# Kernel tuning notes

Measured on AMD Instinct MI355X. Metric: run time of the kernel, lower is better.

The kernel has to match this reference:

```python
import jax, jax.numpy as jnp
import numpy as np

D = 1024       # d_model
S = 32         # n_slots
EMA = 0.05     # slot_ema (alpha)
RSCALE = 1.0   # read_logit_scale
LN_EPS = 1e-5


def setup_inputs() -> dict:
    key = jax.random.key(0)
    ks = jax.random.split(key, 6)
    B, T = 2, 2048
    h = jax.random.normal(ks[0], (B, T, D), jnp.float32)
    # init_batched_memory_state: small random slots
    state0 = jax.random.normal(ks[1], (B, S, D), jnp.float32) * 0.01
    # xavier_uniform for (out=D, in=D) Linear weights, zero bias
    bound = float(np.sqrt(6.0 / (D + D)))
    Wq = jax.random.uniform(ks[2], (D, D), jnp.float32, -bound, bound)
    Wv = jax.random.uniform(ks[3], (D, D), jnp.float32, -bound, bound)
    bq = jnp.zeros((D,), jnp.float32)
    bv = jnp.zeros((D,), jnp.float32)
    ln_gamma = jnp.ones((D,), jnp.float32)
    ln_beta = jnp.zeros((D,), jnp.float32)
    return {"h": h, "state0": state0, "ln_gamma": ln_gamma, "ln_beta": ln_beta,
            "Wq": Wq, "bq": bq, "Wv": Wv, "bv": bv, "chunk_size": 128}


def _layer_norm(x, gamma, beta):
    mu = jnp.mean(x, axis=-1, keepdims=True)
    var = jnp.mean(jnp.square(x - mu), axis=-1, keepdims=True)
    return (x - mu) * jax.lax.rsqrt(var + LN_EPS) * gamma + beta


def reference(h, state0, ln_gamma, ln_beta, Wq, bq, Wv, bv, chunk_size):
    """write_parallel (soft-routed EMA prefix-scan write) followed by
    read_parallel (per-token softmax slot attention). Returns (ctx, final_state)."""
    B, T, d = h.shape
    alpha = EMA
    a = 1.0 - alpha
    h_norm = _layer_norm(h, ln_gamma, ln_beta)                  # (B,T,d)
    v = h_norm @ Wv.T + bv                                      # value_proj
    q = h_norm @ Wq.T + bq                                      # query_proj
    scale = RSCALE * d ** (-0.5)
    # routing weights from queries vs initial state (breaks seq dependency)
    scores = jnp.einsum('btd,bsd->bts', q, state0) * scale       # (B,T,S)
    w = jax.nn.softmax(scores, axis=-1)
    u = alpha * w[..., None] * v[:, :, None, :]                  # (B,T,S,d)

    n_chunks = T // chunk_size
    Cn = chunk_size
    u_chunks = u.reshape(B, n_chunks, Cn, S, d).transpose(1, 0, 2, 3, 4)
    t_idx = jnp.arange(Cn, dtype=h.dtype)
    decay = a ** t_idx                                           # (Cn,)
    inv_decay = 1.0 / jnp.clip(decay, 1e-30)
    t1_decay = a ** (t_idx + 1.0)

    def step(state, u_c):  # state (B,S,d), u_c (B,Cn,S,d)
        cs = jnp.cumsum(u_c * inv_decay[None, :, None, None], axis=1)
        chunk_states = (decay[None, :, None, None] * cs
                        + t1_decay[None, :, None, None] * state[:, None])
        return chunk_states[:, -1], chunk_states

    final_state, states = jax.lax.scan(step, state0, u_chunks)
    states = states.transpose(1, 0, 2, 3, 4).reshape(B, T, S, d)  # (B,T,S,d)

    # read_parallel: softmax slot attention per token against its own state
    scores_r = jnp.einsum('btd,btsd->bts', q, states) * scale
    attn = jax.nn.softmax(scores_r, axis=-1)
    ctx = jnp.einsum('bts,btsd->btd', attn, states)               # (B,T,d)
    return ctx, final_state
```

## Files before the change

kernel.cpp:

```cpp
#include <hip/hip_runtime.h>

#define Bn 2
#define Tn 2048
#define Dn 1024
#define Sn 32
#define CH 64
#define NCH 32
#define ALPHA 0.05f
#define Adec 0.95f
#define SCALE 0.03125f

typedef __attribute__((ext_vector_type(8))) __bf16 bf16x8;
typedef __attribute__((ext_vector_type(4))) __bf16 bf16x4;
typedef __attribute__((ext_vector_type(4))) float f32x4;

__device__ __forceinline__ void async_copy16(const void* g, void* l) {
  __builtin_amdgcn_global_load_lds(
      (const __attribute__((address_space(1))) unsigned int*)g,
      (__attribute__((address_space(3))) unsigned int*)l, 16, 0, 0);
}

__device__ __forceinline__ bool is_bf16(const void* gam) {
  return ((const unsigned short*)gam)[0] == 0x3F80u;
}

#define W8 (Dn * Dn / 8)
#define S8 (Bn * Sn * Dn / 8)
__global__ __launch_bounds__(256) void conv_k(
    const void* __restrict__ Wq, const void* __restrict__ Wv,
    const void* __restrict__ s0, const void* __restrict__ gam,
    __bf16* __restrict__ Wqb, __bf16* __restrict__ Wvb, __bf16* __restrict__ s0b) {
  bool isb = is_bf16(gam);
  int g = blockIdx.x * 256 + threadIdx.x;
  const void* src; __bf16* dst; int off;
  if (g < W8)            { src = Wq; dst = Wqb; off = g; }
  else if (g < 2 * W8)   { src = Wv; dst = Wvb; off = g - W8; }
  else                   { src = s0; dst = s0b; off = g - 2 * W8; }
  if (isb) {
    *(bf16x8*)&dst[(size_t)off * 8] = ((const bf16x8*)src)[off];
  } else {
    const float* s = (const float*)src + (size_t)off * 8;
    f32x4 a = *(const f32x4*)s, b = *(const f32x4*)(s + 4);
    bf16x8 t;
    t[0] = (__bf16)a[0]; t[1] = (__bf16)a[1]; t[2] = (__bf16)a[2]; t[3] = (__bf16)a[3];
    t[4] = (__bf16)b[0]; t[5] = (__bf16)b[1]; t[6] = (__bf16)b[2]; t[7] = (__bf16)b[3];
    *(bf16x8*)&dst[(size_t)off * 8] = t;
  }
}

__global__ __launch_bounds__(256) void ln_k(const void* __restrict__ hp,
    const void* __restrict__ gp, const void* __restrict__ bp,
    __bf16* __restrict__ hn) {
  int row = blockIdx.x;
  int tid = threadIdx.x;
  bool isb = is_bf16(gp);
  float x0, x1, x2, x3;
  if (isb) {
    const __bf16* x = (const __bf16*)hp + (size_t)row * Dn;
    bf16x4 xv = *(const bf16x4*)&x[tid * 4];
    x0 = (float)xv[0]; x1 = (float)xv[1]; x2 = (float)xv[2]; x3 = (float)xv[3];
  } else {
    const float* x = (const float*)hp + (size_t)row * Dn;
    f32x4 xv = *(const f32x4*)&x[tid * 4];
    x0 = xv[0]; x1 = xv[1]; x2 = xv[2]; x3 = xv[3];
  }
  float s  = x0 + x1 + x2 + x3;
  float s2 = x0*x0 + x1*x1 + x2*x2 + x3*x3;
  #pragma unroll
  for (int m = 32; m >= 1; m >>= 1) { s += __shfl_xor(s, m); s2 += __shfl_xor(s2, m); }
  __shared__ float red[8];
  int wave = tid >> 6, lane = tid & 63;
  if (lane == 0) { red[wave] = s; red[4 + wave] = s2; }
  __syncthreads();
  s  = red[0] + red[1] + red[2] + red[3];
  s2 = red[4] + red[5] + red[6] + red[7];
  float mu  = s * (1.0f / Dn);
  float var = s2 * (1.0f / Dn) - mu * mu;
  float rs  = rsqrtf(var + 1e-5f);
  float g0, g1, g2, g3, be0, be1, be2, be3;
  if (isb) {
    bf16x4 gv = *(const bf16x4*)&((const __bf16*)gp)[tid * 4];
    bf16x4 bv = *(const bf16x4*)&((const __bf16*)bp)[tid * 4];
    g0 = (float)gv[0]; g1 = (float)gv[1]; g2 = (float)gv[2]; g3 = (float)gv[3];
    be0 = (float)bv[0]; be1 = (float)bv[1]; be2 = (float)bv[2]; be3 = (float)bv[3];
  } else {
    f32x4 gv = *(const f32x4*)&((const float*)gp)[tid * 4];
    f32x4 bv = *(const f32x4*)&((const float*)bp)[tid * 4];
    g0 = gv[0]; g1 = gv[1]; g2 = gv[2]; g3 = gv[3];
    be0 = bv[0]; be1 = bv[1]; be2 = bv[2]; be3 = bv[3];
  }
  bf16x4 o;
  o[0] = (__bf16)((x0 - mu) * rs * g0 + be0);
  o[1] = (__bf16)((x1 - mu) * rs * g1 + be1);
  o[2] = (__bf16)((x2 - mu) * rs * g2 + be2);
  o[3] = (__bf16)((x3 - mu) * rs * g3 + be3);
  *(bf16x4*)&hn[(size_t)row * Dn + tid * 4] = o;
}

__global__ __launch_bounds__(256) void gemm_qv_k(
    const __bf16* __restrict__ A,
    const __bf16* __restrict__ Wqb, const void* __restrict__ bqp,
    const __bf16* __restrict__ Wvb, const void* __restrict__ bvp,
    const void* __restrict__ gam,
    __bf16* __restrict__ Qo, __bf16* __restrict__ Vo) {
  const int K = Dn, N = Dn;
  bool isb = is_bf16(gam);
  int mt = blockIdx.x & 31;
  int ng = blockIdx.x >> 5;
  const __bf16* W; const void* biasp; __bf16* O; int nt;
  if (ng < 8) { W = Wqb; biasp = bqp; O = Qo; nt = ng; }
  else        { W = Wvb; biasp = bvp; O = Vo; nt = ng - 8; }
  int m0 = mt * 128, n0 = nt * 128;
  __shared__ alignas(16) __bf16 lA[128 * 64];
  __shared__ alignas(16) __bf16 lB[128 * 64];
  int tid = threadIdx.x, lane = tid & 63, wave = tid >> 6;
  int wm = (wave >> 1) * 64, wn = (wave & 1) * 64;
  int lm = lane & 15, q8 = (lane >> 4) * 8;
  f32x4 zero4 = {0.f, 0.f, 0.f, 0.f};
  f32x4 acc[4][4];
  #pragma unroll
  for (int i = 0; i < 4; ++i)
    #pragma unroll
    for (int j = 0; j < 4; ++j) acc[i][j] = zero4;

  for (int k0 = 0; k0 < K; k0 += 64) {
    __syncthreads();
    #pragma unroll
    for (int r = 0; r < 4; ++r) {
      int idx = r * 256 + tid;
      int row = idx >> 3, c8 = (idx & 7) * 8;
      async_copy16(&A[(size_t)(m0 + row) * K + k0 + c8], &lA[idx * 8]);
      async_copy16(&W[(size_t)(n0 + row) * K + k0 + c8], &lB[idx * 8]);
    }
    __syncthreads();
    #pragma unroll
    for (int kk = 0; kk < 64; kk += 32) {
      bf16x8 af[4], bfr[4];
      #pragma unroll
      for (int i = 0; i < 4; ++i) {
        af[i]  = *(const bf16x8*)&lA[(wm + i * 16 + lm) * 64 + kk + q8];
        bfr[i] = *(const bf16x8*)&lB[(wn + i * 16 + lm) * 64 + kk + q8];
      }
      #pragma unroll
      for (int i = 0; i < 4; ++i)
        #pragma unroll
        for (int j = 0; j < 4; ++j)
          acc[i][j] = __builtin_amdgcn_mfma_f32_16x16x32_bf16(af[i], bfr[j], acc[i][j], 0, 0, 0);
    }
  }
  int r4 = (lane >> 4) * 4;
  #pragma unroll
  for (int j = 0; j < 4; ++j) {
    int colN = n0 + wn + j * 16 + lm;
    float bb = isb ? (float)((const __bf16*)biasp)[colN] : ((const float*)biasp)[colN];
    #pragma unroll
    for (int i = 0; i < 4; ++i) {
      int row0 = m0 + wm + i * 16 + r4;
      #pragma unroll
      for (int r = 0; r < 4; ++r)
        O[(size_t)(row0 + r) * N + colN] = (__bf16)(acc[i][j][r] + bb);
    }
  }
}

#define SP 33
__global__ __launch_bounds__(256) void router_k(const __bf16* __restrict__ qb,
    const __bf16* __restrict__ s0b, float* __restrict__ wbuf) {
  int tokBase = blockIdx.x * 64;
  int b = tokBase >> 11;
  const __bf16* S = s0b + (size_t)b * Sn * Dn;
  __shared__ alignas(16) __bf16 lQ[64 * 64];
  __shared__ alignas(16) __bf16 lS[Sn * 64];
  __shared__ float fSc[64 * SP];
  int tid = threadIdx.x, lane = tid & 63, wave = tid >> 6;
  int lm = lane & 15, q8 = (lane >> 4) * 8;
  f32x4 zero4 = {0.f, 0.f, 0.f, 0.f};
  f32x4 acc[2]; acc[0] = zero4; acc[1] = zero4;

  for (int k0 = 0; k0 < Dn; k0 += 64) {
    __syncthreads();
    #pragma unroll
    for (int r = 0; r < 2; ++r) {
      int idx = r * 256 + tid;
      async_copy16(&qb[(size_t)(tokBase + (idx >> 3)) * Dn + k0 + (idx & 7) * 8], &lQ[idx * 8]);
    }
    async_copy16(&S[(size_t)(tid >> 3) * Dn + k0 + (tid & 7) * 8], &lS[tid * 8]);
    __syncthreads();
    #pragma unroll
    for (int kk = 0; kk < 64; kk += 32) {
      bf16x8 af = *(const bf16x8*)&lQ[(wave * 16 + lm) * 64 + kk + q8];
      #pragma unroll
      for (int j = 0; j < 2; ++j) {
        bf16x8 bb = *(const bf16x8*)&lS[(j * 16 + lm) * 64 + kk + q8];
        acc[j] = __builtin_amdgcn_mfma_f32_16x16x32_bf16(af, bb, acc[j], 0, 0, 0);
      }
    }
  }
  int r4 = (lane >> 4) * 4;
  #pragma unroll
  for (int j = 0; j < 2; ++j)
    #pragma unroll
    for (int r = 0; r < 4; ++r)
      fSc[(wave * 16 + r4 + r) * SP + j * 16 + lm] = acc[j][r];
  __syncthreads();
  if (tid < 64) {
    int t = tid;
    float mx = -1e30f;
    #pragma unroll
    for (int s = 0; s < Sn; ++s) mx = fmaxf(mx, fSc[t * SP + s]);
    float sum = 0.f;
    float ex[Sn];
    #pragma unroll
    for (int s = 0; s < Sn; ++s) { ex[s] = __expf(fSc[t * SP + s] * SCALE - mx * SCALE); sum += ex[s]; }
    float inv = 1.f / sum;
    #pragma unroll
    for (int s = 0; s < Sn; ++s)
      wbuf[(size_t)(tokBase + t) * Sn + s] = ex[s] * inv;
  }
}

__global__ __launch_bounds__(256) void contrib_k(const __bf16* __restrict__ v,
    const float* __restrict__ wbuf, float* __restrict__ contrib) {
  int blk = blockIdx.x;
  int bc = blk >> 2, dq = blk & 3;
  int b = bc >> 5, c = bc & 31;
  int tokBase = b * Tn + c * CH;
  int d0 = dq * 256;
  __shared__ alignas(16) float coef[CH * Sn];
  __shared__ float dp[CH];
  int tid = threadIdx.x;
  if (tid < CH) dp[tid] = powf(Adec, (float)(CH - 1 - tid));
  __syncthreads();
  for (int i = tid; i < CH * Sn; i += 256) {
    int j = i >> 5;
    coef[i] = ALPHA * dp[j] * wbuf[(size_t)tokBase * Sn + i];
  }
  __syncthreads();
  int st = tid >> 6;
  int dg = tid & 63;
  int d4 = d0 + dg * 4;
  int sb = st * 8;
  f32x4 zero4 = {0.f, 0.f, 0.f, 0.f};
  f32x4 acc[8];
  #pragma unroll
  for (int i = 0; i < 8; ++i) acc[i] = zero4;
  for (int j = 0; j < CH; ++j) {
    bf16x4 vv = *(const bf16x4*)&v[(size_t)(tokBase + j) * Dn + d4];
    f32x4 vf = {(float)vv[0], (float)vv[1], (float)vv[2], (float)vv[3]};
    f32x4 c0 = *(const f32x4*)&coef[j * Sn + sb];
    f32x4 c1 = *(const f32x4*)&coef[j * Sn + sb + 4];
    acc[0] += vf * c0[0]; acc[1] += vf * c0[1]; acc[2] += vf * c0[2]; acc[3] += vf * c0[3];
    acc[4] += vf * c1[0]; acc[5] += vf * c1[1]; acc[6] += vf * c1[2]; acc[7] += vf * c1[3];
  }
  float* outp = contrib + (size_t)bc * Sn * Dn;
  #pragma unroll
  for (int i = 0; i < 8; ++i)
    *(f32x4*)&outp[(size_t)(sb + i) * Dn + d4] = acc[i];
}

__global__ __launch_bounds__(256) void scan_k(const void* __restrict__ s0p,
    const float* __restrict__ contrib, const void* __restrict__ gam,
    __bf16* __restrict__ S0b, void* __restrict__ outp) {
  int idx = blockIdx.x * 256 + threadIdx.x;
  bool isb = is_bf16(gam);
  int b = idx >> 15, sd = idx & 32767;
  float val = isb ? (float)((const __bf16*)s0p)[idx] : ((const float*)s0p)[idx];
  const float aC = powf(Adec, (float)CH);
  #pragma unroll 8
  for (int c = 0; c < NCH; ++c) {
    size_t off = ((size_t)(b * NCH + c) << 15) + sd;
    S0b[off] = (__bf16)val;
    val = aC * val + contrib[off];
  }
  size_t fsbase = (size_t)Bn * Tn * Dn;
  if (isb) ((__bf16*)outp)[fsbase + idx] = (__bf16)val;
  else     ((float*)outp)[fsbase + idx] = val;
}

__global__ __launch_bounds__(256) void attn_k(
    const __bf16* __restrict__ q, const __bf16* __restrict__ v,
    const float* __restrict__ wbuf, const __bf16* __restrict__ S0b,
    float* __restrict__ Pbuf, float* __restrict__ A2buf) {
  int bc = blockIdx.x;
  int b = bc >> 5, c = bc & 31;
  int tokBase = b * Tn + c * CH;
  const __bf16* S0c = S0b + (size_t)bc * Sn * Dn;

  __shared__ alignas(16) __bf16 lQ[CH * 64];
  __shared__ alignas(16) __bf16 lV[CH * 64];
  __shared__ alignas(16) __bf16 lS[Sn * 64];
  __shared__ alignas(16) __bf16 lM[CH * 72];
  __shared__ alignas(16) __bf16 lW[CH * 40];
  __shared__ alignas(16) __bf16 lWt[Sn * 72];
  __shared__ alignas(16) __bf16 lAt[CH * 40];
  __shared__ float dp[CH + 1];

  int tid = threadIdx.x, lane = tid & 63, wave = tid >> 6;
  int lm = lane & 15, q8 = (lane >> 4) * 8;
  int r4 = (lane >> 4) * 4;
  f32x4 zero4 = {0.f, 0.f, 0.f, 0.f};
  f32x4 aQV[4], aQS[2];
  #pragma unroll
  for (int i = 0; i < 4; ++i) aQV[i] = zero4;
  aQS[0] = zero4; aQS[1] = zero4;

  for (int i = tid; i < CH * Sn; i += 256) {
    int j = i >> 5, s = i & 31;
    __bf16 wb = (__bf16)wbuf[(size_t)tokBase * Sn + i];
    lW[j * 40 + s] = wb;
    lWt[s * 72 + j] = wb;
  }
  if (tid < CH + 1) dp[tid] = powf(Adec, (float)tid);

  for (int k0 = 0; k0 < Dn; k0 += 64) {
    __syncthreads();
    #pragma unroll
    for (int r = 0; r < 2; ++r) {
      int idx = r * 256 + tid;
      int row = idx >> 3, c8 = (idx & 7) * 8;
      async_copy16(&q[(size_t)(tokBase + row) * Dn + k0 + c8], &lQ[idx * 8]);
      async_copy16(&v[(size_t)(tokBase + row) * Dn + k0 + c8], &lV[idx * 8]);
    }
    async_copy16(&S0c[(size_t)(tid >> 3) * Dn + k0 + (tid & 7) * 8], &lS[tid * 8]);
    __syncthreads();
    #pragma unroll
    for (int kk = 0; kk < 64; kk += 32) {
      bf16x8 af = *(const bf16x8*)&lQ[(wave * 16 + lm) * 64 + kk + q8];
      #pragma unroll
      for (int j = 0; j < 4; ++j) {
        bf16x8 bb = *(const bf16x8*)&lV[(j * 16 + lm) * 64 + kk + q8];
        aQV[j] = __builtin_amdgcn_mfma_f32_16x16x32_bf16(af, bb, aQV[j], 0, 0, 0);
      }
      #pragma unroll
      for (int j = 0; j < 2; ++j) {
        bf16x8 bb = *(const bf16x8*)&lS[(j * 16 + lm) * 64 + kk + q8];
        aQS[j] = __builtin_amdgcn_mfma_f32_16x16x32_bf16(af, bb, aQS[j], 0, 0, 0);
      }
    }
  }

  #pragma unroll
  for (int jt = 0; jt < 4; ++jt)
    #pragma unroll
    for (int r = 0; r < 4; ++r) {
      int t = wave * 16 + r4 + r, j = jt * 16 + lm;
      float f = (j <= t) ? ALPHA * dp[t - j] : 0.0f;
      lM[t * 72 + j] = (__bf16)(aQV[jt][r] * f);
    }

  f32x4 sc[2]; sc[0] = zero4; sc[1] = zero4;
  #pragma unroll
  for (int kt = 0; kt < 2; ++kt) {
    bf16x8 am = *(const bf16x8*)&lM[(wave * 16 + lm) * 72 + kt * 32 + q8];
    #pragma unroll
    for (int st = 0; st < 2; ++st) {
      bf16x8 bb = *(const bf16x8*)&lWt[(st * 16 + lm) * 72 + kt * 32 + q8];
      sc[st] = __builtin_amdgcn_mfma_f32_16x16x32_bf16(am, bb, sc[st], 0, 0, 0);
    }
  }
  float at0[4], at1[4];
  #pragma unroll
  for (int r = 0; r < 4; ++r) {
    int t = wave * 16 + r4 + r;
    float aQ = dp[t - wave * 16 + 1 + wave * 16];
    float s0v = SCALE * (aQ * aQS[0][r] + sc[0][r]);
    float s1v = SCALE * (aQ * aQS[1][r] + sc[1][r]);
    float mx = fmaxf(s0v, s1v);
    #pragma unroll
    for (int m = 8; m >= 1; m >>= 1) mx = fmaxf(mx, __shfl_xor(mx, m));
    float e0 = __expf(s0v - mx), e1 = __expf(s1v - mx);
    float su = e0 + e1;
    #pragma unroll
    for (int m = 8; m >= 1; m >>= 1) su += __shfl_xor(su, m);
    float inv = 1.f / su;
    at0[r] = e0 * inv; at1[r] = e1 * inv;
    A2buf[(size_t)bc * CH * Sn + t * Sn + lm]      = aQ * at0[r];
    A2buf[(size_t)bc * CH * Sn + t * Sn + 16 + lm] = aQ * at1[r];
    lAt[t * 40 + lm]      = (__bf16)at0[r];
    lAt[t * 40 + 16 + lm] = (__bf16)at1[r];
  }
  bf16x8 aa = *(const bf16x8*)&lAt[(wave * 16 + lm) * 40 + q8];
  #pragma unroll
  for (int jt = 0; jt < 4; ++jt) {
    bf16x8 bb = *(const bf16x8*)&lW[(jt * 16 + lm) * 40 + q8];
    f32x4 pj = __builtin_amdgcn_mfma_f32_16x16x32_bf16(aa, bb, zero4, 0, 0, 0);
    #pragma unroll
    for (int r = 0; r < 4; ++r) {
      int t = wave * 16 + r4 + r, j = jt * 16 + lm;
      float val = (j <= t) ? ALPHA * dp[t - j] * pj[r] : 0.0f;
      Pbuf[(size_t)bc * CH * CH + t * CH + j] = val;
    }
  }
}

__global__ __launch_bounds__(256) void ctx_k(const __bf16* __restrict__ v,
    const __bf16* __restrict__ S0b, const float* __restrict__ Pbuf,
    const float* __restrict__ A2buf, const void* __restrict__ gam,
    void* __restrict__ ctxp) {
  int blk = blockIdx.x;
  int bc = blk >> 3, dt = blk & 7;
  int b = bc >> 5, c = bc & 31;
  int tokBase = b * Tn + c * CH;
  int d0 = dt * 128;
  bool isb = is_bf16(gam);
  __shared__ alignas(16) float lP[CH * CH];
  __shared__ alignas(16) float lA2[CH * Sn];
  __shared__ alignas(16) __bf16 lV[CH * 128];
  __shared__ alignas(16) __bf16 lS[Sn * 128];
  int tid = threadIdx.x;
  {
    const f32x4* src = (const f32x4*)(Pbuf + (size_t)bc * CH * CH);
    f32x4* dst = (f32x4*)lP;
    for (int i = tid; i < CH * CH / 4; i += 256) dst[i] = src[i];
    const f32x4* src2 = (const f32x4*)(A2buf + (size_t)bc * CH * Sn);
    f32x4* dst2 = (f32x4*)lA2;
    for (int i = tid; i < CH * Sn / 4; i += 256) dst2[i] = src2[i];
    for (int i = tid; i < CH * 128 / 8; i += 256) {
      int j = i >> 4, dd = (i & 15) * 8;
      *(bf16x8*)&lV[j * 128 + dd] = *(const bf16x8*)&v[(size_t)(tokBase + j) * Dn + d0 + dd];
    }
    for (int i = tid; i < Sn * 128 / 8; i += 256) {
      int s = i >> 4, dd = (i & 15) * 8;
      *(bf16x8*)&lS[s * 128 + dd] = *(const bf16x8*)&S0b[((size_t)bc * Sn + s) * Dn + d0 + dd];
    }
  }
  __syncthreads();
  int tt = tid >> 5, dg = tid & 31;
  int t0 = tt * 8, d4 = dg * 4;
  f32x4 zero4 = {0.f, 0.f, 0.f, 0.f};
  f32x4 acc[8];
  #pragma unroll
  for (int i = 0; i < 8; ++i) acc[i] = zero4;
  for (int j4 = 0; j4 < CH; j4 += 4) {
    f32x4 vf[4];
    #pragma unroll
    for (int k = 0; k < 4; ++k) {
      bf16x4 vv = *(const bf16x4*)&lV[(j4 + k) * 128 + d4];
      vf[k] = f32x4{(float)vv[0], (float)vv[1], (float)vv[2], (float)vv[3]};
    }
    #pragma unroll
    for (int i = 0; i < 8; ++i) {
      f32x4 pr = *(const f32x4*)&lP[(t0 + i) * CH + j4];
      acc[i] += vf[0] * pr[0]; acc[i] += vf[1] * pr[1];
      acc[i] += vf[2] * pr[2]; acc[i] += vf[3] * pr[3];
    }
  }
  for (int s4 = 0; s4 < Sn; s4 += 4) {
    f32x4 sf[4];
    #pragma unroll
    for (int k = 0; k < 4; ++k) {
      bf16x4 sv = *(const bf16x4*)&lS[(s4 + k) * 128 + d4];
      sf[k] = f32x4{(float)sv[0], (float)sv[1], (float)sv[2], (float)sv[3]};
    }
    #pragma unroll
    for (int i = 0; i < 8; ++i) {
      f32x4 ar = *(const f32x4*)&lA2[(t0 + i) * Sn + s4];
      acc[i] += sf[0] * ar[0]; acc[i] += sf[1] * ar[1];
      acc[i] += sf[2] * ar[2]; acc[i] += sf[3] * ar[3];
    }
  }
  if (isb) {
    __bf16* ctx = (__bf16*)ctxp;
    #pragma unroll
    for (int i = 0; i < 8; ++i) {
      bf16x4 o;
      o[0] = (__bf16)acc[i][0]; o[1] = (__bf16)acc[i][1];
      o[2] = (__bf16)acc[i][2]; o[3] = (__bf16)acc[i][3];
      *(bf16x4*)&ctx[(size_t)(tokBase + t0 + i) * Dn + d0 + d4] = o;
    }
  } else {
    float* ctx = (float*)ctxp;
    #pragma unroll
    for (int i = 0; i < 8; ++i)
      *(f32x4*)&ctx[(size_t)(tokBase + t0 + i) * Dn + d0 + d4] = acc[i];
  }
}

extern "C" void kernel_launch(void* const* d_in, const int* in_sizes, int n_in,
                              void* d_out, int out_size, void* d_ws, size_t ws_size,
                              hipStream_t stream) {
  (void)in_sizes; (void)n_in; (void)out_size; (void)ws_size;
  const void* h      = d_in[0];
  const void* state0 = d_in[1];
  const void* gam    = d_in[2];
  const void* bet    = d_in[3];
  const void* Wq     = d_in[4];
  const void* bq     = d_in[5];
  const void* Wv     = d_in[6];
  const void* bv     = d_in[7];

  char* ws = (char*)d_ws;
  __bf16* hn      = (__bf16*)(ws);
  __bf16* qb      = (__bf16*)(ws + (8u << 20));
  __bf16* vb      = (__bf16*)(ws + (16u << 20));
  float*  wbuf    = (float*)(ws + (24u << 20));
  float*  contrib = (float*)(ws + (25u << 20));
  __bf16* S0b     = (__bf16*)(ws + (34u << 20));
  float*  Pbuf    = (float*)(ws + (43u << 20));
  float*  A2buf   = (float*)(ws + (45u << 20));
  __bf16* Wqb     = (__bf16*)(ws + (47u << 20));
  __bf16* Wvb     = (__bf16*)(ws + (49u << 20));
  __bf16* s0b     = (__bf16*)(ws + (51u << 20));

  conv_k<<<(2 * W8 + S8) / 256, 256, 0, stream>>>(Wq, Wv, state0, gam, Wqb, Wvb, s0b);
  ln_k<<<Bn * Tn, 256, 0, stream>>>(h, gam, bet, hn);
  gemm_qv_k<<<512, 256, 0, stream>>>(hn, Wqb, bq, Wvb, bv, gam, qb, vb);
  router_k<<<Bn * Tn / 64, 256, 0, stream>>>(qb, s0b, wbuf);
  contrib_k<<<Bn * NCH * 4, 256, 0, stream>>>(vb, wbuf, contrib);
  scan_k<<<Bn * Sn * Dn / 256, 256, 0, stream>>>(state0, contrib, gam, S0b, d_out);
  attn_k<<<Bn * NCH, 256, 0, stream>>>(qb, vb, wbuf, S0b, Pbuf, A2buf);
  ctx_k<<<Bn * NCH * 8, 256, 0, stream>>>(vb, S0b, Pbuf, A2buf, gam, d_out);
}
```

Baseline: 184.1 us.

## Merge conversion into LayerNorm kernel, split-K router, and preload scan contributions

Three changes. The weight/state conversion kernel and the LayerNorm kernel become one launch, with extra blocks doing the conversion. The router now handles 16 tokens per block with split-K across waves, reading directly from global memory instead of staging through LDS. The waves' partial sums are reduced in shared memory and the softmax is computed with shuffles across 256 threads. The scan kernel loads all 32 chunk contributions into registers before the recurrence, so the loads can be in flight together, at the cost of higher register pressure.

```diff
diff --git a/kernel.cpp b/kernel.cpp
--- a/kernel.cpp
+++ b/kernel.cpp
@@ -26,34 +26,33 @@
 
 #define W8 (Dn * Dn / 8)
 #define S8 (Bn * Sn * Dn / 8)
-__global__ __launch_bounds__(256) void conv_k(
-    const void* __restrict__ Wq, const void* __restrict__ Wv,
-    const void* __restrict__ s0, const void* __restrict__ gam,
-    __bf16* __restrict__ Wqb, __bf16* __restrict__ Wvb, __bf16* __restrict__ s0b) {
-  bool isb = is_bf16(gam);
-  int g = blockIdx.x * 256 + threadIdx.x;
-  const void* src; __bf16* dst; int off;
-  if (g < W8)            { src = Wq; dst = Wqb; off = g; }
-  else if (g < 2 * W8)   { src = Wv; dst = Wvb; off = g - W8; }
-  else                   { src = s0; dst = s0b; off = g - 2 * W8; }
-  if (isb) {
-    *(bf16x8*)&dst[(size_t)off * 8] = ((const bf16x8*)src)[off];
-  } else {
-    const float* s = (const float*)src + (size_t)off * 8;
-    f32x4 a = *(const f32x4*)s, b = *(const f32x4*)(s + 4);
-    bf16x8 t;
-    t[0] = (__bf16)a[0]; t[1] = (__bf16)a[1]; t[2] = (__bf16)a[2]; t[3] = (__bf16)a[3];
-    t[4] = (__bf16)b[0]; t[5] = (__bf16)b[1]; t[6] = (__bf16)b[2]; t[7] = (__bf16)b[3];
-    *(bf16x8*)&dst[(size_t)off * 8] = t;
-  }
-}
-
-__global__ __launch_bounds__(256) void ln_k(const void* __restrict__ hp,
-    const void* __restrict__ gp, const void* __restrict__ bp,
-    __bf16* __restrict__ hn) {
+#define LNB (Bn * Tn)
+__global__ __launch_bounds__(256) void prep_k(
+    const void* __restrict__ hp, const void* __restrict__ gp, const void* __restrict__ bp,
+    const void* __restrict__ Wq, const void* __restrict__ Wv, const void* __restrict__ s0,
+    __bf16* __restrict__ hn, __bf16* __restrict__ Wqb, __bf16* __restrict__ Wvb,
+    __bf16* __restrict__ s0b) {
+  bool isb = is_bf16(gp);
+  int tid = threadIdx.x;
+  if (blockIdx.x >= LNB) {
+    int g = (blockIdx.x - LNB) * 256 + tid;
+    const void* src; __bf16* dst; int off;
+    if (g < W8)            { src = Wq; dst = Wqb; off = g; }
+    else if (g < 2 * W8)   { src = Wv; dst = Wvb; off = g - W8; }
+    else                   { src = s0; dst = s0b; off = g - 2 * W8; }
+    if (isb) {
+      *(bf16x8*)&dst[(size_t)off * 8] = ((const bf16x8*)src)[off];
+    } else {
+      const float* s = (const float*)src + (size_t)off * 8;
+      f32x4 a = *(const f32x4*)s, b = *(const f32x4*)(s + 4);
+      bf16x8 t;
+      t[0] = (__bf16)a[0]; t[1] = (__bf16)a[1]; t[2] = (__bf16)a[2]; t[3] = (__bf16)a[3];
+      t[4] = (__bf16)b[0]; t[5] = (__bf16)b[1]; t[6] = (__bf16)b[2]; t[7] = (__bf16)b[3];
+      *(bf16x8*)&dst[(size_t)off * 8] = t;
+    }
+    return;
+  }
   int row = blockIdx.x;
-  int tid = threadIdx.x;
-  bool isb = is_bf16(gp);
   float x0, x1, x2, x3;
   if (isb) {
     const __bf16* x = (const __bf16*)hp + (size_t)row * Dn;
@@ -163,60 +162,48 @@
   }
 }
 
-#define SP 33
 __global__ __launch_bounds__(256) void router_k(const __bf16* __restrict__ qb,
     const __bf16* __restrict__ s0b, float* __restrict__ wbuf) {
-  int tokBase = blockIdx.x * 64;
+  int tokBase = blockIdx.x * 16;
   int b = tokBase >> 11;
-  const __bf16* S = s0b + (size_t)b * Sn * Dn;
-  __shared__ alignas(16) __bf16 lQ[64 * 64];
-  __shared__ alignas(16) __bf16 lS[Sn * 64];
-  __shared__ float fSc[64 * SP];
   int tid = threadIdx.x, lane = tid & 63, wave = tid >> 6;
   int lm = lane & 15, q8 = (lane >> 4) * 8;
+  const __bf16* qrow = qb + (size_t)(tokBase + lm) * Dn + q8;
+  const __bf16* s0r  = s0b + ((size_t)b * Sn + lm) * Dn + q8;
+  const __bf16* s1r  = s0r + (size_t)16 * Dn;
   f32x4 zero4 = {0.f, 0.f, 0.f, 0.f};
-  f32x4 acc[2]; acc[0] = zero4; acc[1] = zero4;
-
-  for (int k0 = 0; k0 < Dn; k0 += 64) {
-    __syncthreads();
-    #pragma unroll
-    for (int r = 0; r < 2; ++r) {
-      int idx = r * 256 + tid;
-      async_copy16(&qb[(size_t)(tokBase + (idx >> 3)) * Dn + k0 + (idx & 7) * 8], &lQ[idx * 8]);
-    }
-    async_copy16(&S[(size_t)(tid >> 3) * Dn + k0 + (tid & 7) * 8], &lS[tid * 8]);
-    __syncthreads();
-    #pragma unroll
-    for (int kk = 0; kk < 64; kk += 32) {
-      bf16x8 af = *(const bf16x8*)&lQ[(wave * 16 + lm) * 64 + kk + q8];
-      #pragma unroll
-      for (int j = 0; j < 2; ++j) {
-        bf16x8 bb = *(const bf16x8*)&lS[(j * 16 + lm) * 64 + kk + q8];
-        acc[j] = __builtin_amdgcn_mfma_f32_16x16x32_bf16(af, bb, acc[j], 0, 0, 0);
-      }
-    }
-  }
+  f32x4 acc0 = zero4, acc1 = zero4;
+  #pragma unroll
+  for (int ks = 0; ks < 8; ++ks) {
+    int k0 = wave * 256 + ks * 32;
+    bf16x8 af = *(const bf16x8*)&qrow[k0];
+    bf16x8 b0 = *(const bf16x8*)&s0r[k0];
+    bf16x8 b1 = *(const bf16x8*)&s1r[k0];
+    acc0 = __builtin_amdgcn_mfma_f32_16x16x32_bf16(af, b0, acc0, 0, 0, 0);
+    acc1 = __builtin_amdgcn_mfma_f32_16x16x32_bf16(af, b1, acc1, 0, 0, 0);
+  }
+  __shared__ float red[4][16][33];
   int r4 = (lane >> 4) * 4;
   #pragma unroll
-  for (int j = 0; j < 2; ++j)
-    #pragma unroll
-    for (int r = 0; r < 4; ++r)
-      fSc[(wave * 16 + r4 + r) * SP + j * 16 + lm] = acc[j][r];
+  for (int r = 0; r < 4; ++r) {
+    red[wave][r4 + r][lm]      = acc0[r];
+    red[wave][r4 + r][lm + 16] = acc1[r];
+  }
   __syncthreads();
-  if (tid < 64) {
-    int t = tid;
-    float mx = -1e30f;
-    #pragma unroll
-    for (int s = 0; s < Sn; ++s) mx = fmaxf(mx, fSc[t * SP + s]);
-    float sum = 0.f;
-    float ex[Sn];
-    #pragma unroll
-    for (int s = 0; s < Sn; ++s) { ex[s] = __expf(fSc[t * SP + s] * SCALE - mx * SCALE); sum += ex[s]; }
-    float inv = 1.f / sum;
-    #pragma unroll
-    for (int s = 0; s < Sn; ++s)
-      wbuf[(size_t)(tokBase + t) * Sn + s] = ex[s] * inv;
-  }
+  int t = tid >> 4, s = tid & 15;
+  float sc0 = (red[0][t][s]      + red[1][t][s])      + (red[2][t][s]      + red[3][t][s]);
+  float sc1 = (red[0][t][s + 16] + red[1][t][s + 16]) + (red[2][t][s + 16] + red[3][t][s + 16]);
+  sc0 *= SCALE; sc1 *= SCALE;
+  float mx = fmaxf(sc0, sc1);
+  #pragma unroll
+  for (int m = 8; m >= 1; m >>= 1) mx = fmaxf(mx, __shfl_xor(mx, m));
+  float e0 = __expf(sc0 - mx), e1 = __expf(sc1 - mx);
+  float su = e0 + e1;
+  #pragma unroll
+  for (int m = 8; m >= 1; m >>= 1) su += __shfl_xor(su, m);
+  float inv = 1.f / su;
+  wbuf[(size_t)(tokBase + t) * Sn + s]      = e0 * inv;
+  wbuf[(size_t)(tokBase + t) * Sn + s + 16] = e1 * inv;
 }
 
 __global__ __launch_bounds__(256) void contrib_k(const __bf16* __restrict__ v,
@@ -266,11 +253,14 @@
   int b = idx >> 15, sd = idx & 32767;
   float val = isb ? (float)((const __bf16*)s0p)[idx] : ((const float*)s0p)[idx];
   const float aC = powf(Adec, (float)CH);
-  #pragma unroll 8
+  float cv[NCH];
+  #pragma unroll
+  for (int c = 0; c < NCH; ++c)
+    cv[c] = contrib[((size_t)(b * NCH + c) << 15) + sd];
+  #pragma unroll
   for (int c = 0; c < NCH; ++c) {
-    size_t off = ((size_t)(b * NCH + c) << 15) + sd;
-    S0b[off] = (__bf16)val;
-    val = aC * val + contrib[off];
+    S0b[((size_t)(b * NCH + c) << 15) + sd] = (__bf16)val;
+    val = aC * val + cv[c];
   }
   size_t fsbase = (size_t)Bn * Tn * Dn;
   if (isb) ((__bf16*)outp)[fsbase + idx] = (__bf16)val;
@@ -362,7 +352,7 @@
   #pragma unroll
   for (int r = 0; r < 4; ++r) {
     int t = wave * 16 + r4 + r;
-    float aQ = dp[t - wave * 16 + 1 + wave * 16];
+    float aQ = dp[t + 1];
     float s0v = SCALE * (aQ * aQS[0][r] + sc[0][r]);
     float s1v = SCALE * (aQ * aQS[1][r] + sc[1][r]);
     float mx = fmaxf(s0v, s1v);
@@ -502,10 +492,11 @@
   __bf16* Wvb     = (__bf16*)(ws + (49u << 20));
   __bf16* s0b     = (__bf16*)(ws + (51u << 20));
 
-  conv_k<<<(2 * W8 + S8) / 256, 256, 0, stream>>>(Wq, Wv, state0, gam, Wqb, Wvb, s0b);
-  ln_k<<<Bn * Tn, 256, 0, stream>>>(h, gam, bet, hn);
+  int convBlocks = (2 * W8 + S8) / 256;
+  prep_k<<<LNB + convBlocks, 256, 0, stream>>>(h, gam, bet, Wq, Wv, state0,
+                                               hn, Wqb, Wvb, s0b);
   gemm_qv_k<<<512, 256, 0, stream>>>(hn, Wqb, bq, Wvb, bv, gam, qb, vb);
-  router_k<<<Bn * Tn / 64, 256, 0, stream>>>(qb, s0b, wbuf);
+  router_k<<<Bn * Tn / 16, 256, 0, stream>>>(qb, s0b, wbuf);
   contrib_k<<<Bn * NCH * 4, 256, 0, stream>>>(vb, wbuf, contrib);
   scan_k<<<Bn * Sn * Dn / 256, 256, 0, stream>>>(state0, contrib, gam, S0b, d_out);
   attn_k<<<Bn * NCH, 256, 0, stream>>>(qb, vb, wbuf, S0b, Pbuf, A2buf);
```

After: 176.6 us. -4.1%, faster.
